# Kernel optimization log

Hardware: AMD Instinct MI355X
Metric: run time of the kernel (lower is better)

Reference implementation:

```python
import jax, jax.numpy as jnp
import numpy as np
import math

B, S, DM = 2, 2048, 2048
NH, NKV, HD = 16, 4, 128
DFF = 8192
K_KEEP = DFF // 2  # sparsity_ratio = 0.5
EPS = 1e-6


def setup_inputs() -> dict:
    key = jax.random.key(0)
    ks = jax.random.split(key, 10)
    sc = 0.02
    return {
        "hidden_states": jax.random.normal(ks[0], (B, S, DM), dtype=jnp.float32),
        "wq": jax.random.normal(ks[1], (NH * HD, DM), dtype=jnp.float32) * sc,
        "wk": jax.random.normal(ks[2], (NKV * HD, DM), dtype=jnp.float32) * sc,
        "wv": jax.random.normal(ks[3], (NKV * HD, DM), dtype=jnp.float32) * sc,
        "wo": jax.random.normal(ks[4], (DM, NH * HD), dtype=jnp.float32) * sc,
        "ln1_w": jnp.ones((DM,), dtype=jnp.float32),
        "ln2_w": jnp.ones((DM,), dtype=jnp.float32),
        "w_gate": jax.random.normal(ks[5], (DFF, DM), dtype=jnp.float32) * sc,
        "w_up": jax.random.normal(ks[6], (DFF, DM), dtype=jnp.float32) * sc,
        "w_down": jax.random.normal(ks[7], (DM, DFF), dtype=jnp.float32) * sc,
    }


def _rmsnorm(x, w):
    var = jnp.mean(x * x, axis=-1, keepdims=True)
    return x * jax.lax.rsqrt(var + EPS) * w


def reference(hidden_states, wq, wk, wv, wo, ln1_w, ln2_w, w_gate, w_up, w_down):
    b, s, _ = hidden_states.shape
    # --- attention sub-block: RMSNorm -> GQA causal attention -> residual ---
    x = _rmsnorm(hidden_states, ln1_w)
    q = (x @ wq.T).reshape(b, s, NH, HD)
    k = (x @ wk.T).reshape(b, s, NKV, HD)
    v = (x @ wv.T).reshape(b, s, NKV, HD)
    # expand KV heads to match query heads (GQA)
    rep = NH // NKV
    k = jnp.repeat(k, rep, axis=2)
    v = jnp.repeat(v, rep, axis=2)
    scores = jnp.einsum('bqhd,bkhd->bhqk', q, k) / math.sqrt(HD)
    causal = jnp.tril(jnp.ones((s, s), dtype=bool))
    scores = jnp.where(causal, scores, jnp.finfo(scores.dtype).min)
    attn = jax.nn.softmax(scores, axis=-1)
    o = jnp.einsum('bhqk,bkhd->bqhd', attn, v).reshape(b, s, NH * HD)
    h = hidden_states + o @ wo.T
    # --- FFN sub-block: RMSNorm -> TopK-sparse SwiGLU -> residual ---
    y = _rmsnorm(h, ln2_w)
    gate = jax.nn.silu(y @ w_gate.T)  # [b, s, DFF]
    mag = jnp.abs(gate)
    thr = jax.lax.top_k(mag, K_KEEP)[0][..., -1:]  # kth-largest magnitude
    gate = jnp.where(mag >= thr, gate, 0.0)
    ff = (gate * (y @ w_up.T)) @ w_down.T
    return h + ff
```

## Files before the change

kernel.cpp:

```cpp
#include <hip/hip_runtime.h>
#include <stdint.h>

constexpr int SEQ    = 2048;
constexpr int DMODEL = 2048;
constexpr int NHEADS = 16;
constexpr int NKVH   = 4;
constexpr int HDIM   = 128;
constexpr int DFFN   = 8192;
constexpr int BATCH  = 2;
constexpr int MTOK   = BATCH * SEQ;
constexpr int KKEEP  = DFFN / 2;

typedef __bf16 bf16x8 __attribute__((ext_vector_type(8)));
typedef float  f32x4  __attribute__((ext_vector_type(4)));
typedef float  f32x16 __attribute__((ext_vector_type(16)));
typedef unsigned short u16;
typedef unsigned int   u32;

__device__ __forceinline__ u16 f2bu(float f) {
  u32 x = __builtin_bit_cast(u32, f);
  return (u16)((x + 0x7FFFu + ((x >> 16) & 1u)) >> 16);
}
__device__ __forceinline__ float b2f(u16 u) {
  u32 v = ((u32)u) << 16;
  return __builtin_bit_cast(float, v);
}
__device__ __forceinline__ void gl_lds16(const void* g, void* l) {
  __builtin_amdgcn_global_load_lds((const __attribute__((address_space(1))) u32*)g,
                                   (__attribute__((address_space(3))) u32*)l, 16, 0, 0);
}

__global__ __launch_bounds__(256) void cvt_kernel(const float* __restrict__ in,
                                                  u16* __restrict__ out, int n) {
  int i = (blockIdx.x * 256 + threadIdx.x) * 4;
  if (i >= n) return;
  float4 v = *(const float4*)(in + i);
  uint2 pk;
  pk.x = (u32)f2bu(v.x) | ((u32)f2bu(v.y) << 16);
  pk.y = (u32)f2bu(v.z) | ((u32)f2bu(v.w) << 16);
  *(uint2*)(out + i) = pk;
}

__global__ __launch_bounds__(256) void rmsnorm_kernel(const float* __restrict__ in,
                                                      const float* __restrict__ w,
                                                      u16* __restrict__ out) {
  const int tid = threadIdx.x;
  const size_t row = blockIdx.x;
  const float* x = in + row * DMODEL;
  float4 v0 = *(const float4*)(x + tid * 4);
  float4 v1 = *(const float4*)(x + 1024 + tid * 4);
  float s = v0.x*v0.x + v0.y*v0.y + v0.z*v0.z + v0.w*v0.w
          + v1.x*v1.x + v1.y*v1.y + v1.z*v1.z + v1.w*v1.w;
#pragma unroll
  for (int off = 1; off < 64; off <<= 1) s += __shfl_xor(s, off, 64);
  __shared__ float wsum[4];
  if ((tid & 63) == 0) wsum[tid >> 6] = s;
  __syncthreads();
  s = wsum[0] + wsum[1] + wsum[2] + wsum[3];
  const float rinv = rsqrtf(s * (1.0f / DMODEL) + 1e-6f);
  u16* o = out + row * DMODEL;
#pragma unroll
  for (int part = 0; part < 2; ++part) {
    int c = part * 1024 + tid * 4;
    float4 vv = (part == 0) ? v0 : v1;
    float4 wv = *(const float4*)(w + c);
    uint2 pk;
    pk.x = (u32)f2bu(vv.x * rinv * wv.x) | ((u32)f2bu(vv.y * rinv * wv.y) << 16);
    pk.y = (u32)f2bu(vv.z * rinv * wv.z) | ((u32)f2bu(vv.w * rinv * wv.w) << 16);
    *(uint2*)(o + c) = pk;
  }
}

template <int EPI>
__global__ __launch_bounds__(256, 2)
void gemm_bt(const u16* __restrict__ A, const u16* __restrict__ B,
             void* __restrict__ C, const float* res,
             int M, int N, int K) {
  __shared__ u16 As[2][128 * 64];
  __shared__ u16 Bs[2][128 * 64];
  const int tid = threadIdx.x;
  const int wave = tid >> 6, lane = tid & 63;
  const int nwg = gridDim.x * gridDim.y;
  const int lin = blockIdx.y * gridDim.x + blockIdx.x;
  const int swz = (lin & 7) * (nwg >> 3) + (lin >> 3);
  const int m0 = (swz / gridDim.x) * 128, n0 = (swz % gridDim.x) * 128;
  const int r_in = lane >> 3, chk = lane & 7;
  const int fk = lane >> 4, fc = lane & 15;
  const int wm = (wave >> 1) * 64, wn = (wave & 1) * 64;
  const int nt = K >> 6;
  f32x4 acc[4][4] = {};

  auto stage = [&](int buf, int t) {
    const int kt = t * 64;
#pragma unroll
    for (int i = 0; i < 4; ++i) {
      int row = wave * 32 + i * 8 + r_in;
      int gc = chk ^ (row & 7);
      gl_lds16(A + (size_t)(m0 + row) * K + kt + gc * 8, &As[buf][(wave * 32 + i * 8) * 64]);
    }
#pragma unroll
    for (int i = 0; i < 4; ++i) {
      int row = wave * 32 + i * 8 + r_in;
      int gc = chk ^ (row & 7);
      gl_lds16(B + (size_t)(n0 + row) * K + kt + gc * 8, &Bs[buf][(wave * 32 + i * 8) * 64]);
    }
  };

  stage(0, 0);
  asm volatile("s_waitcnt vmcnt(0)" ::: "memory");
  __builtin_amdgcn_s_barrier();

  for (int t = 0; t < nt; ++t) {
    if (t + 1 < nt) stage((t + 1) & 1, t + 1);
    const u16* Ab = As[t & 1];
    const u16* Bb = Bs[t & 1];
#pragma unroll
    for (int kk = 0; kk < 2; ++kk) {
      bf16x8 a[4], b[4];
#pragma unroll
      for (int i = 0; i < 4; ++i) {
        int row = wm + i * 16 + fc;
        int c = (kk * 4 + fk) ^ (row & 7);
        a[i] = *(const bf16x8*)(Ab + row * 64 + c * 8);
      }
#pragma unroll
      for (int j = 0; j < 4; ++j) {
        int row = wn + j * 16 + fc;
        int c = (kk * 4 + fk) ^ (row & 7);
        b[j] = *(const bf16x8*)(Bb + row * 64 + c * 8);
      }
#pragma unroll
      for (int i = 0; i < 4; ++i)
#pragma unroll
        for (int j = 0; j < 4; ++j)
          acc[i][j] = __builtin_amdgcn_mfma_f32_16x16x32_bf16(a[i], b[j], acc[i][j], 0, 0, 0);
    }
    asm volatile("s_waitcnt vmcnt(0)" ::: "memory");
    __builtin_amdgcn_s_barrier();
  }

  const int rb = fk * 4;
#pragma unroll
  for (int i = 0; i < 4; ++i) {
#pragma unroll
    for (int j = 0; j < 4; ++j) {
      int row = m0 + wm + i * 16 + rb;
      int col = n0 + wn + j * 16 + fc;
      f32x4 v = acc[i][j];
      if constexpr (EPI == 0) {
        u16* o = (u16*)C;
#pragma unroll
        for (int r = 0; r < 4; ++r) o[(size_t)(row + r) * N + col] = f2bu(v[r]);
      } else if constexpr (EPI == 1) {
        u16* o = (u16*)C;
        int bb = row >> 11, s = row & (SEQ - 1);
        int kvh = col >> 7, d = col & (HDIM - 1);
        size_t base = (((size_t)bb * NKVH + kvh) * HDIM + d) * SEQ + s;
        uint2 pk;
        pk.x = (u32)f2bu(v[0]) | ((u32)f2bu(v[1]) << 16);
        pk.y = (u32)f2bu(v[2]) | ((u32)f2bu(v[3]) << 16);
        *(uint2*)(o + base) = pk;
      } else if constexpr (EPI == 2) {
        float* o = (float*)C;
#pragma unroll
        for (int r = 0; r < 4; ++r) {
          size_t idx = (size_t)(row + r) * N + col;
          float rv = res[idx];
          o[idx] = v[r] + rv;
        }
      } else {
        float* o = (float*)C;
#pragma unroll
        for (int r = 0; r < 4; ++r) {
          float g = v[r];
          o[(size_t)(row + r) * N + col] = g / (1.0f + __expf(-g));
        }
      }
    }
  }
}

__global__ __launch_bounds__(256, 2)
void attn_kernel(const u16* __restrict__ Q, const u16* __restrict__ Kb,
                 const u16* __restrict__ Vt, u16* __restrict__ O) {
  __shared__ u16 Ksh[2 * 32 * 128];
  __shared__ u16 Vsh[2 * 128 * 32];
  const int tid = threadIdx.x, wave = tid >> 6, lane = tid & 63;
  const int half = lane >> 5, l31 = lane & 31;
  const int d_lin = blockIdx.x + gridDim.x * (blockIdx.y + gridDim.y * blockIdx.z);
  const int lin = (d_lin & 7) * 64 + (d_lin >> 3);
  const int bx = lin & 15, h = (lin >> 4) & 15, b = lin >> 8;
  const int kvh = h >> 2;
  const int qw = bx * 128 + wave * 32;
  const float SC = 0.08838834764831845f;
  const int ntb = bx * 4 + 4;
  const int nmy = bx * 4 + wave;

  bf16x8 qf[8];
  {
    const u16* qp = Q + ((size_t)(b * SEQ + qw + l31)) * DMODEL + h * HDIM + half * 8;
#pragma unroll
    for (int s = 0; s < 8; ++s) qf[s] = *(const bf16x8*)(qp + s * 16);
  }
  f32x16 oacc[4] = {};
  float m_run = -1e30f, l_run = 0.0f;
  const size_t vbase = ((size_t)(b * NKVH + kvh)) * HDIM * SEQ;
  const u16* kbase = Kb + (size_t)b * SEQ * (NKVH * HDIM) + kvh * HDIM;

  auto stage = [&](int bi, int k0) {
    u16* Kd = Ksh + bi * 4096;
    u16* Vd = Vsh + bi * 4096;
#pragma unroll
    for (int ii = 0; ii < 2; ++ii) {
      int inst = wave * 2 + ii;
      {
        int row = inst * 4 + (lane >> 4);
        int c = (lane & 15) ^ (row & 15);
        gl_lds16(kbase + (size_t)(k0 + row) * (NKVH * HDIM) + c * 8, Kd + inst * 512);
      }
      {
        int row = inst * 16 + (lane >> 2);
        int c = (lane & 3) ^ ((row >> 1) & 3);
        gl_lds16(Vt + vbase + (size_t)row * SEQ + k0 + c * 8, Vd + inst * 512);
      }
    }
  };

  stage(0, 0);
  __syncthreads();

  for (int t = 0; t < ntb; ++t) {
    if (t + 1 < ntb) stage((t + 1) & 1, (t + 1) * 32);
    if (t <= nmy) {
      const u16* Kd = Ksh + (t & 1) * 4096;
      const u16* Vd = Vsh + (t & 1) * 4096;
      f32x16 st = {};
#pragma unroll
      for (int s = 0; s < 8; ++s) {
        int c = (half + 2 * s) ^ (l31 & 15);
        bf16x8 kf = *(const bf16x8*)(Kd + l31 * 128 + c * 8);
        st = __builtin_amdgcn_mfma_f32_32x32x16_bf16(kf, qf[s], st, 0, 0, 0);
      }
      const bool diag = (t * 32 == qw);
      float sv[16];
#pragma unroll
      for (int r = 0; r < 16; ++r) {
        float x = st[r] * SC;
        if (diag) {
          int kvl = (r & 3) + 8 * (r >> 2) + 4 * half;
          if (kvl > l31) x = -1e30f;
        }
        sv[r] = x;
      }
      float mx = sv[0];
#pragma unroll
      for (int r = 1; r < 16; ++r) mx = fmaxf(mx, sv[r]);
      mx = fmaxf(mx, __shfl_xor(mx, 32, 64));
      if (__any(mx > m_run + 4.0f)) {
        float mnew = fmaxf(m_run, mx);
        float alpha = __expf(m_run - mnew);
        m_run = mnew;
        l_run *= alpha;
#pragma unroll
        for (int r = 0; r < 16; ++r) {
          float ar = __shfl(alpha, (r & 3) + 8 * (r >> 2) + 4 * half, 64);
#pragma unroll
          for (int dt = 0; dt < 4; ++dt) oacc[dt][r] *= ar;
        }
      }
      float p[16];
      float rs = 0.0f;
#pragma unroll
      for (int r = 0; r < 16; ++r) { p[r] = __expf(sv[r] - m_run); rs += p[r]; }
      rs += __shfl_xor(rs, 32, 64);
      l_run += rs;
      u32 c01 = (u32)f2bu(p[0])  | ((u32)f2bu(p[1])  << 16);
      u32 c23 = (u32)f2bu(p[2])  | ((u32)f2bu(p[3])  << 16);
      u32 c45 = (u32)f2bu(p[4])  | ((u32)f2bu(p[5])  << 16);
      u32 c67 = (u32)f2bu(p[6])  | ((u32)f2bu(p[7])  << 16);
      u32 c89 = (u32)f2bu(p[8])  | ((u32)f2bu(p[9])  << 16);
      u32 cAB = (u32)f2bu(p[10]) | ((u32)f2bu(p[11]) << 16);
      u32 cCD = (u32)f2bu(p[12]) | ((u32)f2bu(p[13]) << 16);
      u32 cEF = (u32)f2bu(p[14]) | ((u32)f2bu(p[15]) << 16);
      u32 paw[2][4];
      {
        u32 sA = __shfl_xor(c01, 32, 64), sB = __shfl_xor(c23, 32, 64);
        u32 sC = __shfl_xor(c45, 32, 64), sD = __shfl_xor(c67, 32, 64);
        paw[0][0] = half ? sC : c01;  paw[0][1] = half ? sD : c23;
        paw[0][2] = half ? c45 : sA;  paw[0][3] = half ? c67 : sB;
      }
      {
        u32 sA = __shfl_xor(c89, 32, 64), sB = __shfl_xor(cAB, 32, 64);
        u32 sC = __shfl_xor(cCD, 32, 64), sD = __shfl_xor(cEF, 32, 64);
        paw[1][0] = half ? sC : c89;  paw[1][1] = half ? sD : cAB;
        paw[1][2] = half ? cCD : sA;  paw[1][3] = half ? cEF : sB;
      }
#pragma unroll
      for (int ks = 0; ks < 2; ++ks) {
        bf16x8 paf = __builtin_bit_cast(bf16x8, *(uint4*)&paw[ks][0]);
#pragma unroll
        for (int dt = 0; dt < 4; ++dt) {
          int row = dt * 32 + l31;
          int c = (half + 2 * ks) ^ ((row >> 1) & 3);
          bf16x8 vf = *(const bf16x8*)(Vd + row * 32 + c * 8);
          oacc[dt] = __builtin_amdgcn_mfma_f32_32x32x16_bf16(paf, vf, oacc[dt], 0, 0, 0);
        }
      }
    }
    __syncthreads();
  }

  float rinv = 1.0f / l_run;
  u16* ob = O + ((size_t)(b * SEQ + qw)) * DMODEL + h * HDIM + l31;
#pragma unroll
  for (int r = 0; r < 16; ++r) {
    int qr = (r & 3) + 8 * (r >> 2) + 4 * half;
    float ir = __shfl(rinv, qr, 64);
#pragma unroll
    for (int dt = 0; dt < 4; ++dt)
      ob[(size_t)qr * DMODEL + dt * 32] = f2bu(oacc[dt][r] * ir);
  }
}

__global__ __launch_bounds__(256)
void topk_kernel(const float* __restrict__ gate, u16* __restrict__ upact) {
  __shared__ u32 sabs[DFFN];
  __shared__ u32 hist[4][256];
  __shared__ u32 ss[257];
  __shared__ u32 sh_prefix, sh_rem;
  const int tid = threadIdx.x, wave = tid >> 6;
  const size_t row = blockIdx.x;
  const float* g = gate + row * DFFN;
  for (int it = 0; it < 4; ++it) {
    int e = it * 2048 + tid * 8;
    float4 a = *(const float4*)(g + e);
    float4 b = *(const float4*)(g + e + 4);
    sabs[e + 0] = __builtin_bit_cast(u32, a.x);
    sabs[e + 1] = __builtin_bit_cast(u32, a.y);
    sabs[e + 2] = __builtin_bit_cast(u32, a.z);
    sabs[e + 3] = __builtin_bit_cast(u32, a.w);
    sabs[e + 4] = __builtin_bit_cast(u32, b.x);
    sabs[e + 5] = __builtin_bit_cast(u32, b.y);
    sabs[e + 6] = __builtin_bit_cast(u32, b.z);
    sabs[e + 7] = __builtin_bit_cast(u32, b.w);
  }
  if (tid == 0) { sh_prefix = 0; sh_rem = KKEEP; }
  __syncthreads();
  for (int pass = 0; pass < 4; ++pass) {
    const int p = 24 - pass * 8;
    const u32 mask_hi = (pass == 0) ? 0u : (0xFFFFFFFFu << (p + 8));
    for (int i = tid; i < 1024; i += 256) ((u32*)hist)[i] = 0;
    __syncthreads();
    const u32 prefix = sh_prefix, rem = sh_rem;
    for (int it = 0; it < 4; ++it) {
      int e = it * 2048 + tid * 8;
#pragma unroll
      for (int j = 0; j < 8; ++j) {
        u32 mg = sabs[e + j] & 0x7FFFFFFFu;
        if ((mg & mask_hi) == (prefix & mask_hi))
          atomicAdd(&hist[wave][(mg >> p) & 0xFF], 1u);
      }
    }
    __syncthreads();
    ss[tid] = hist[0][tid] + hist[1][tid] + hist[2][tid] + hist[3][tid];
    if (tid == 0) ss[256] = 0;
    __syncthreads();
    for (int off = 1; off < 256; off <<= 1) {
      u32 v = (tid + off < 256) ? ss[tid + off] : 0u;
      __syncthreads();
      ss[tid] += v;
      __syncthreads();
    }
    if (ss[tid] >= rem && ss[tid + 1] < rem) {
      sh_prefix = prefix | ((u32)tid << p);
      sh_rem = rem - ss[tid + 1];
    }
    __syncthreads();
  }
  const u32 thr = sh_prefix;
  u16* ua = upact + row * DFFN;
  for (int it = 0; it < 4; ++it) {
    int e = it * 2048 + tid * 8;
    uint4 uv = *(const uint4*)(ua + e);
    const u16* up16 = (const u16*)&uv;
    u16 outp[8];
#pragma unroll
    for (int j = 0; j < 8; ++j) {
      u32 bits = sabs[e + j];
      u32 mg = bits & 0x7FFFFFFFu;
      float gg = __builtin_bit_cast(float, bits);
      float prod = (mg >= thr) ? gg * b2f(up16[j]) : 0.0f;
      outp[j] = f2bu(prod);
    }
    uint4 ov;
    ov.x = (u32)outp[0] | ((u32)outp[1] << 16);
    ov.y = (u32)outp[2] | ((u32)outp[3] << 16);
    ov.z = (u32)outp[4] | ((u32)outp[5] << 16);
    ov.w = (u32)outp[6] | ((u32)outp[7] << 16);
    *(uint4*)(ua + e) = ov;
  }
}

extern "C" void kernel_launch(void* const* d_in, const int* in_sizes, int n_in,
                              void* d_out, int out_size, void* d_ws, size_t ws_size,
                              hipStream_t stream) {
  const float* hidden = (const float*)d_in[0];
  const float* wq = (const float*)d_in[1];
  const float* wk = (const float*)d_in[2];
  const float* wv = (const float*)d_in[3];
  const float* wo = (const float*)d_in[4];
  const float* ln1 = (const float*)d_in[5];
  const float* ln2 = (const float*)d_in[6];
  const float* wg = (const float*)d_in[7];
  const float* wu = (const float*)d_in[8];
  const float* wd = (const float*)d_in[9];
  float* out = (float*)d_out;
  (void)in_sizes; (void)n_in; (void)out_size;

  size_t off = 0;
  auto alloc = [&](size_t n) { char* r = (char*)d_ws + off; off += (n + 255) & ~(size_t)255; return r; };
  u16* wq_b = (u16*)alloc((size_t)DMODEL * DMODEL * 2);
  u16* wk_b = (u16*)alloc((size_t)NKVH * HDIM * DMODEL * 2);
  u16* wv_b = (u16*)alloc((size_t)NKVH * HDIM * DMODEL * 2);
  u16* wo_b = (u16*)alloc((size_t)DMODEL * DMODEL * 2);
  u16* wg_b = (u16*)alloc((size_t)DFFN * DMODEL * 2);
  u16* tok  = (u16*)alloc((size_t)MTOK * DMODEL * 2);
  u16* upb  = (u16*)alloc((size_t)MTOK * DFFN * 2);
  char* S   = alloc((size_t)(MTOK / 2) * DFFN * 4);
  u16* qb   = (u16*)S;
  u16* kb   = (u16*)(S + (size_t)MTOK * DMODEL * 2);
  u16* vtb  = (u16*)(S + (size_t)MTOK * DMODEL * 2 + (size_t)MTOK * NKVH * HDIM * 2);
  u16* wu_b = (u16*)(S + (size_t)MTOK * DMODEL * 2 + 2 * (size_t)MTOK * NKVH * HDIM * 2);
  float* gateh = (float*)S;
  u16* wd_b = (u16*)S;
  const size_t needed = off;
  if (ws_size < needed) return;

  auto cvt = [&](const float* src, u16* dst, size_t n) {
    cvt_kernel<<<dim3((unsigned)(n / 1024)), 256, 0, stream>>>(src, dst, (int)n);
  };
  cvt(wq, wq_b, (size_t)DMODEL * DMODEL);
  cvt(wk, wk_b, (size_t)NKVH * HDIM * DMODEL);
  cvt(wv, wv_b, (size_t)NKVH * HDIM * DMODEL);
  cvt(wo, wo_b, (size_t)DMODEL * DMODEL);
  cvt(wg, wg_b, (size_t)DFFN * DMODEL);
  cvt(wu, wu_b, (size_t)DFFN * DMODEL);

  rmsnorm_kernel<<<MTOK, 256, 0, stream>>>(hidden, ln1, tok);

  gemm_bt<0><<<dim3(DMODEL / 128, MTOK / 128), 256, 0, stream>>>(
      tok, wq_b, qb, nullptr, MTOK, DMODEL, DMODEL);
  gemm_bt<0><<<dim3(NKVH * HDIM / 128, MTOK / 128), 256, 0, stream>>>(
      tok, wk_b, kb, nullptr, MTOK, NKVH * HDIM, DMODEL);
  gemm_bt<1><<<dim3(NKVH * HDIM / 128, MTOK / 128), 256, 0, stream>>>(
      tok, wv_b, vtb, nullptr, MTOK, NKVH * HDIM, DMODEL);

  attn_kernel<<<dim3(SEQ / 128, NHEADS, BATCH), 256, 0, stream>>>(qb, kb, vtb, tok);

  gemm_bt<2><<<dim3(DMODEL / 128, MTOK / 128), 256, 0, stream>>>(
      tok, wo_b, out, hidden, MTOK, DMODEL, DMODEL);

  rmsnorm_kernel<<<MTOK, 256, 0, stream>>>(out, ln2, tok);

  gemm_bt<0><<<dim3(DFFN / 128, MTOK / 128), 256, 0, stream>>>(
      tok, wu_b, upb, nullptr, MTOK, DFFN, DMODEL);

  for (int half = 0; half < 2; ++half) {
    const u16* yh = tok + (size_t)half * (MTOK / 2) * DMODEL;
    u16* uph = upb + (size_t)half * (MTOK / 2) * DFFN;
    gemm_bt<3><<<dim3(DFFN / 128, (MTOK / 2) / 128), 256, 0, stream>>>(
        yh, wg_b, gateh, nullptr, MTOK / 2, DFFN, DMODEL);
    topk_kernel<<<MTOK / 2, 256, 0, stream>>>(gateh, uph);
  }

  cvt(wd, wd_b, (size_t)DMODEL * DFFN);

  gemm_bt<2><<<dim3(DMODEL / 128, MTOK / 128), 256, 0, stream>>>(
      upb, wd_b, out, out, MTOK, DMODEL, DFFN);
}
```

Before: 1.045 ms.

## Add 256x256-tile GEMM kernel for up and gate projections

Adds a new 512-thread GEMM kernel that computes 256x256 output tiles. It uses double-buffered LDS staging with swizzled layout, split A loads interleaved with MFMA phases, grid swizzling, and priority raising around the MFMA blocks. The kernel replaces the 128x128 GEMM for the FFN up and gate projections, aiming for more data reuse per loaded tile and higher MFMA utilisation. In exchange it needs more registers for the 8x4 accumulators, and the large M=2048 gate halves give fewer workgroups, which could underfill the GPU.

```diff
diff --git a/kernel.cpp b/kernel.cpp
--- a/kernel.cpp
+++ b/kernel.cpp
@@ -168,6 +168,118 @@
           float rv = res[idx];
           o[idx] = v[r] + rv;
         }
+      } else {
+        float* o = (float*)C;
+#pragma unroll
+        for (int r = 0; r < 4; ++r) {
+          float g = v[r];
+          o[(size_t)(row + r) * N + col] = g / (1.0f + __expf(-g));
+        }
+      }
+    }
+  }
+}
+
+template <int EPI>
+__global__ __launch_bounds__(512, 2)
+void gemm256(const u16* __restrict__ A, const u16* __restrict__ B,
+             void* __restrict__ C, int M, int N, int K) {
+  __shared__ u16 As[2][2][128 * 32];
+  __shared__ u16 Bs[2][2][128 * 32];
+  const int tid = threadIdx.x;
+  const int wave = tid >> 6, lane = tid & 63;
+  const int nwg = gridDim.x * gridDim.y;
+  const int lin = blockIdx.y * gridDim.x + blockIdx.x;
+  const int swz = (lin & 7) * (nwg >> 3) + (lin >> 3);
+  const int m0 = (swz / gridDim.x) * 256, n0 = (swz % gridDim.x) * 256;
+  const int wm = wave >> 2, wn = wave & 3;
+  const int fk = lane >> 4, fc = lane & 15;
+  const int nt = K >> 5;
+  const int s_row = (wave * 64 + lane) >> 2;
+  const int s_gc = (lane & 3) ^ ((s_row >> 1) & 3);
+  f32x4 acc[8][4] = {};
+
+  auto stageA = [&](int buf, int t) {
+    const int kt = t * 32;
+#pragma unroll
+    for (int h = 0; h < 2; ++h)
+      gl_lds16(A + (size_t)(m0 + h * 128 + s_row) * K + kt + s_gc * 8,
+               &As[buf][h][wave * 512]);
+  };
+  auto stageB = [&](int buf, int t) {
+    const int kt = t * 32;
+#pragma unroll
+    for (int h = 0; h < 2; ++h)
+      gl_lds16(B + (size_t)(n0 + h * 128 + s_row) * K + kt + s_gc * 8,
+               &Bs[buf][h][wave * 512]);
+  };
+
+  stageA(0, 0); stageB(0, 0);
+  asm volatile("s_waitcnt vmcnt(0)" ::: "memory");
+  __builtin_amdgcn_s_barrier();
+
+  for (int t = 0; t < nt; ++t) {
+    const int buf = t & 1, nxt = buf ^ 1;
+    const u16* Ab = &As[buf][wm][0];
+    const u16* Bb = &Bs[buf][wn >> 1][0];
+    bf16x8 a[4], b[4];
+    if (t + 1 < nt) stageA(nxt, t + 1);
+#pragma unroll
+    for (int n = 0; n < 4; ++n) {
+      int row = (wn & 1) * 64 + n * 16 + fc;
+      int slot = fk ^ ((row >> 1) & 3);
+      b[n] = *(const bf16x8*)(Bb + row * 32 + slot * 8);
+    }
+#pragma unroll
+    for (int m = 0; m < 4; ++m) {
+      int row = m * 16 + fc;
+      int slot = fk ^ ((row >> 1) & 3);
+      a[m] = *(const bf16x8*)(Ab + row * 32 + slot * 8);
+    }
+    __builtin_amdgcn_s_barrier();
+    asm volatile("s_waitcnt lgkmcnt(0)" ::: "memory");
+    __builtin_amdgcn_sched_barrier(0);
+    __builtin_amdgcn_s_setprio(1);
+#pragma unroll
+    for (int m = 0; m < 4; ++m)
+#pragma unroll
+      for (int n = 0; n < 4; ++n)
+        acc[m][n] = __builtin_amdgcn_mfma_f32_16x16x32_bf16(a[m], b[n], acc[m][n], 0, 0, 0);
+    __builtin_amdgcn_s_setprio(0);
+    __builtin_amdgcn_s_barrier();
+    if (t + 1 < nt) stageB(nxt, t + 1);
+#pragma unroll
+    for (int m = 0; m < 4; ++m) {
+      int row = (m + 4) * 16 + fc;
+      int slot = fk ^ ((row >> 1) & 3);
+      a[m] = *(const bf16x8*)(Ab + row * 32 + slot * 8);
+    }
+    __builtin_amdgcn_s_barrier();
+    asm volatile("s_waitcnt lgkmcnt(0)" ::: "memory");
+    __builtin_amdgcn_sched_barrier(0);
+    __builtin_amdgcn_s_setprio(1);
+#pragma unroll
+    for (int m = 0; m < 4; ++m)
+#pragma unroll
+      for (int n = 0; n < 4; ++n)
+        acc[m + 4][n] = __builtin_amdgcn_mfma_f32_16x16x32_bf16(a[m], b[n], acc[m + 4][n], 0, 0, 0);
+    __builtin_amdgcn_s_setprio(0);
+    if (t + 1 < nt) asm volatile("s_waitcnt vmcnt(0)" ::: "memory");
+    __builtin_amdgcn_s_barrier();
+  }
+
+  const int rb = fk * 4;
+#pragma unroll
+  for (int m = 0; m < 8; ++m) {
+#pragma unroll
+    for (int n = 0; n < 4; ++n) {
+      int row = m0 + wm * 128 + m * 16 + rb;
+      int col = n0 + wn * 64 + n * 16 + fc;
+      f32x4 v = acc[m][n];
+      if constexpr (EPI == 0) {
+        u16* o = (u16*)C;
+#pragma unroll
+        for (int r = 0; r < 4; ++r) o[(size_t)(row + r) * N + col] = f2bu(v[r]);
       } else {
         float* o = (float*)C;
 #pragma unroll
@@ -462,14 +574,14 @@
 
   rmsnorm_kernel<<<MTOK, 256, 0, stream>>>(out, ln2, tok);
 
-  gemm_bt<0><<<dim3(DFFN / 128, MTOK / 128), 256, 0, stream>>>(
-      tok, wu_b, upb, nullptr, MTOK, DFFN, DMODEL);
+  gemm256<0><<<dim3(DFFN / 256, MTOK / 256), 512, 0, stream>>>(
+      tok, wu_b, upb, MTOK, DFFN, DMODEL);
 
   for (int half = 0; half < 2; ++half) {
     const u16* yh = tok + (size_t)half * (MTOK / 2) * DMODEL;
     u16* uph = upb + (size_t)half * (MTOK / 2) * DFFN;
-    gemm_bt<3><<<dim3(DFFN / 128, (MTOK / 2) / 128), 256, 0, stream>>>(
-        yh, wg_b, gateh, nullptr, MTOK / 2, DFFN, DMODEL);
+    gemm256<3><<<dim3(DFFN / 256, (MTOK / 2) / 256), 512, 0, stream>>>(
+        yh, wg_b, gateh, MTOK / 2, DFFN, DMODEL);
     topk_kernel<<<MTOK / 2, 256, 0, stream>>>(gateh, uph);
   }
 
```

Result: slower. 1.104 ms (+5.7%).
